# Kernel optimization log

Hardware: AMD Instinct MI355X
Metric: run time of the kernel (lower is better)

The kernel has to match this reference:

```python
import jax, jax.numpy as jnp
import numpy as np

NUM_EMBEDDINGS = 1024
EMBEDDING_DIM = 64
COMMITMENT_COST = 0.25


def setup_inputs() -> dict:
    key = jax.random.key(0)
    k_in, k_w = jax.random.split(key)
    inputs = jax.random.normal(k_in, (32, 64, 32, 32), dtype=jnp.float32)
    # nn.Embedding weight initialized uniform(-1/K, 1/K)
    bound = 1.0 / NUM_EMBEDDINGS
    weight = jax.random.uniform(k_w, (NUM_EMBEDDINGS, EMBEDDING_DIM),
                                dtype=jnp.float32, minval=-bound, maxval=bound)
    return {"inputs": inputs, "weight": weight}


def reference(inputs, weight):
    # Flatten to [N, D] rows in embedding space
    flat = inputs.reshape(-1, EMBEDDING_DIM)  # [N, D]
    distances = (jnp.sum(flat * flat, axis=1, keepdims=True)
                 + jnp.sum(weight * weight, axis=1)
                 - 2.0 * jnp.matmul(flat, weight.T))
    encoding_indices = jnp.argmin(distances, axis=1)  # [N]
    quantized = weight[encoding_indices].reshape(inputs.shape)
    e_latent_loss = jnp.mean((jax.lax.stop_gradient(quantized) - inputs) ** 2)
    q_latent_loss = jnp.mean((quantized - jax.lax.stop_gradient(inputs)) ** 2)
    commitment_loss = COMMITMENT_COST * (q_latent_loss + e_latent_loss)
    # Straight-through estimator
    quantized = inputs + jax.lax.stop_gradient(quantized - inputs)
    return quantized, encoding_indices[:, None], commitment_loss
```

## Files before the change

### kernel.cpp

```cpp
#include <hip/hip_runtime.h>

#define NROWS  32768
#define DIM    64
#define KCODES 1024
#define NELEM  (NROWS * DIM)
#define CHUNKS 16
#define CPC    (KCODES / CHUNKS)

typedef float v2f __attribute__((ext_vector_type(2)));

__device__ __forceinline__ float np_sumsq64(const float v[64]) {
#pragma clang fp contract(off)
  float r0 = v[0] * v[0];
  float r1 = v[1] * v[1];
  float r2 = v[2] * v[2];
  float r3 = v[3] * v[3];
  float r4 = v[4] * v[4];
  float r5 = v[5] * v[5];
  float r6 = v[6] * v[6];
  float r7 = v[7] * v[7];
#pragma unroll
  for (int i = 8; i < 64; i += 8) {
    r0 += v[i + 0] * v[i + 0];
    r1 += v[i + 1] * v[i + 1];
    r2 += v[i + 2] * v[i + 2];
    r3 += v[i + 3] * v[i + 3];
    r4 += v[i + 4] * v[i + 4];
    r5 += v[i + 5] * v[i + 5];
    r6 += v[i + 6] * v[i + 6];
    r7 += v[i + 7] * v[i + 7];
  }
  return ((r0 + r1) + (r2 + r3)) + ((r4 + r5) + (r6 + r7));
}

__global__ __launch_bounds__(256) void vq_prep(const float* __restrict__ x,
                                               const float* __restrict__ w,
                                               float* __restrict__ se,
                                               float* __restrict__ sxv,
                                               unsigned long long* __restrict__ keys) {
  const int t = blockIdx.x * 256 + threadIdx.x;
  keys[t] = ~0ull;

  float v[64];
  const float4* xr = (const float4*)(x + (size_t)t * DIM);
#pragma unroll
  for (int i = 0; i < 16; ++i) {
    float4 q = xr[i];
    v[4 * i + 0] = q.x; v[4 * i + 1] = q.y;
    v[4 * i + 2] = q.z; v[4 * i + 3] = q.w;
  }
  sxv[t] = np_sumsq64(v);

  if (t < KCODES) {
    const float4* wr = (const float4*)(w + (size_t)t * DIM);
#pragma unroll
    for (int i = 0; i < 16; ++i) {
      float4 q = wr[i];
      v[4 * i + 0] = q.x; v[4 * i + 1] = q.y;
      v[4 * i + 2] = q.z; v[4 * i + 3] = q.w;
    }
    se[t] = np_sumsq64(v);
  }
}

__global__ __launch_bounds__(256, 4) void vq_dist(const float* __restrict__ x,
                                                  const float* __restrict__ w,
                                                  const float* __restrict__ se,
                                                  const float* __restrict__ sxv,
                                                  unsigned long long* __restrict__ keys) {
  const int bid = blockIdx.x;
  const int l = (bid & 7) * (2048 / 8) + (bid >> 3);
  const int g = l >> 4;
  const int chunk = l & 15;
  const int row = g * 256 + threadIdx.x;

  v2f xv[32];
  const float4* xr = (const float4*)(x + (size_t)row * DIM);
#pragma unroll
  for (int i = 0; i < 16; ++i) {
    float4 t = xr[i];
    xv[2 * i + 0] = (v2f){t.x, t.y};
    xv[2 * i + 1] = (v2f){t.z, t.w};
  }
#pragma unroll
  for (int i = 0; i < 32; ++i) asm volatile("" : "+v"(xv[i]));
  const float sx = sxv[row];

  const int c0 = chunk * CPC;
  const float4* w4 = (const float4*)w;
  float bd = __builtin_inff();
  int bc = 0;

#pragma unroll 2
  for (int j = 0; j < CPC; ++j) {
    const int c = c0 + j;
    const float4* wr = w4 + (size_t)c * 16;
    v2f a0 = (v2f){0.f, 0.f}, a1 = (v2f){0.f, 0.f};
    v2f a2 = (v2f){0.f, 0.f}, a3 = (v2f){0.f, 0.f};
#pragma unroll
    for (int i = 0; i < 16; i += 2) {
      float4 t0 = wr[i];
      float4 t1 = wr[i + 1];
      a0 += (v2f){t0.x, t0.y} * xv[2 * i + 0];
      a1 += (v2f){t0.z, t0.w} * xv[2 * i + 1];
      a2 += (v2f){t1.x, t1.y} * xv[2 * i + 2];
      a3 += (v2f){t1.z, t1.w} * xv[2 * i + 3];
    }
    v2f s01 = a0 + a1;
    v2f s23 = a2 + a3;
    v2f s = s01 + s23;
    float dot = s.x + s.y;
    float d = fmaf(-2.0f, dot, sx + se[c]);
    if (d < bd) { bd = d; bc = c; }
  }

  unsigned long long key =
      ((unsigned long long)__float_as_uint(bd) << 32) | (unsigned long long)(unsigned)bc;
  atomicMin(&keys[row], key);
}

__global__ __launch_bounds__(256) void vq_out(const float* __restrict__ x,
                                              const float* __restrict__ w,
                                              const unsigned long long* __restrict__ keys,
                                              float* __restrict__ outq,
                                              float* __restrict__ outidx,
                                              double* __restrict__ part) {
  __shared__ int sidx[32];
  __shared__ double sp[4];
  const int b = blockIdx.x, t = threadIdx.x;

  if (t < 32) {
    const int row = b * 32 + t;
    unsigned long long k = keys[row];
    const int idx = (int)(unsigned int)(k & 0xFFFFFFFFull);
    outidx[row] = (float)idx;
    sidx[t] = idx;
  }
  __syncthreads();

  double acc = 0.0;
  const float4* x4 = (const float4*)x;
  float4* o4 = (float4*)outq;
#pragma unroll
  for (int i = 0; i < 2; ++i) {
    const int e = i * 256 + t;
    const int rl = e >> 4;
    const int d4 = e & 15;
    const size_t gofs = ((size_t)b * 32 + rl) * 16 + d4;
    float4 xvv = x4[gofs];
    const float4* wr = (const float4*)(w + (size_t)sidx[rl] * DIM);
    float4 wv = wr[d4];
    float tx = wv.x - xvv.x, ty = wv.y - xvv.y;
    float tz = wv.z - xvv.z, tw = wv.w - xvv.w;
    float4 q;
    q.x = xvv.x + tx; q.y = xvv.y + ty;
    q.z = xvv.z + tz; q.w = xvv.w + tw;
    o4[gofs] = q;
    acc += (double)tx * tx + (double)ty * ty + (double)tz * tz + (double)tw * tw;
  }

#pragma unroll
  for (int s = 32; s > 0; s >>= 1) acc += __shfl_down(acc, s, 64);
  if ((t & 63) == 0) sp[t >> 6] = acc;
  __syncthreads();
  if (t == 0) part[b] = (sp[0] + sp[1]) + (sp[2] + sp[3]);
}

__global__ __launch_bounds__(256) void vq_fin(const double* __restrict__ part,
                                              float* __restrict__ outloss) {
  __shared__ double sp[4];
  const int t = threadIdx.x;
  double a = (part[t] + part[t + 256]) + (part[t + 512] + part[t + 768]);
#pragma unroll
  for (int s = 32; s > 0; s >>= 1) a += __shfl_down(a, s, 64);
  if ((t & 63) == 0) sp[t >> 6] = a;
  __syncthreads();
  if (t == 0) {
    double total = (sp[0] + sp[1]) + (sp[2] + sp[3]);
    *outloss = 0.5f * (float)(total / (double)NELEM);
  }
}

extern "C" void kernel_launch(void* const* d_in, const int* in_sizes, int n_in,
                              void* d_out, int out_size, void* d_ws, size_t ws_size,
                              hipStream_t stream) {
  const float* x = (const float*)d_in[0];
  const float* w = (const float*)d_in[1];

  float* outq    = (float*)d_out;
  float* outidx  = outq + NELEM;
  float* outloss = outidx + NROWS;

  char* wsb = (char*)d_ws;
  float* se    = (float*)wsb;
  double* part = (double*)(wsb + 4096);
  float* sxv   = (float*)(wsb + 12288);
  unsigned long long* keys = (unsigned long long*)(wsb + 147456);

  hipLaunchKernelGGL(vq_prep, dim3(128),  dim3(256), 0, stream, x, w, se, sxv, keys);
  hipLaunchKernelGGL(vq_dist, dim3(2048), dim3(256), 0, stream, x, w, se, sxv, keys);
  hipLaunchKernelGGL(vq_out,  dim3(1024), dim3(256), 0, stream, x, w, keys, outq, outidx, part);
  hipLaunchKernelGGL(vq_fin,  dim3(1),    dim3(256), 0, stream, part, outloss);
}
```

Before: 126.0 us.

## Split each row across lane pairs in distance kernel and fuse loss finalization

The distance kernel now gives each row to two adjacent lanes, each holding half of the 64-dim vector, and combines the partial dot products with a DPP pair swap. This halves per-thread register use so launch bounds can allow 8 blocks per SIMD, and the codebook is cut into 8 chunks instead of 16 while keeping the same grid size. The separate final reduction kernel is dropped: each output block atomically adds its partial loss, and the last block, found with an atomic counter, writes the result. The trade-offs are an extra cross-lane op per code and a loss sum whose floating-point addition order is no longer fixed.

```diff
diff --git a/kernel.cpp b/kernel.cpp
--- a/kernel.cpp
+++ b/kernel.cpp
@@ -4,7 +4,7 @@
 #define DIM    64
 #define KCODES 1024
 #define NELEM  (NROWS * DIM)
-#define CHUNKS 16
+#define CHUNKS 8
 #define CPC    (KCODES / CHUNKS)
 
 typedef float v2f __attribute__((ext_vector_type(2)));
@@ -33,12 +33,20 @@
   return ((r0 + r1) + (r2 + r3)) + ((r4 + r5) + (r6 + r7));
 }
 
+__device__ __forceinline__ float swap_pair(float v) {
+  return __int_as_float(
+      __builtin_amdgcn_mov_dpp(__float_as_int(v), 0xB1, 0xF, 0xF, true));
+}
+
 __global__ __launch_bounds__(256) void vq_prep(const float* __restrict__ x,
                                                const float* __restrict__ w,
                                                float* __restrict__ se,
                                                float* __restrict__ sxv,
-                                               unsigned long long* __restrict__ keys) {
+                                               unsigned long long* __restrict__ keys,
+                                               double* __restrict__ loss,
+                                               unsigned int* __restrict__ cnt) {
   const int t = blockIdx.x * 256 + threadIdx.x;
+  if (t == 0) { *loss = 0.0; *cnt = 0u; }
   keys[t] = ~0ull;
 
   float v[64];
@@ -63,60 +71,62 @@
   }
 }
 
-__global__ __launch_bounds__(256, 4) void vq_dist(const float* __restrict__ x,
+__global__ __launch_bounds__(256, 8) void vq_dist(const float* __restrict__ x,
                                                   const float* __restrict__ w,
                                                   const float* __restrict__ se,
                                                   const float* __restrict__ sxv,
                                                   unsigned long long* __restrict__ keys) {
   const int bid = blockIdx.x;
-  const int l = (bid & 7) * (2048 / 8) + (bid >> 3);
-  const int g = l >> 4;
-  const int chunk = l & 15;
-  const int row = g * 256 + threadIdx.x;
-
-  v2f xv[32];
+  const int xcd = bid & 7;
+  const int j = bid >> 3;
+  const int chunk = (j >> 3) & 7;
+  const int group = (xcd << 5) + (j & 7) + ((j >> 6) << 3);
+  const int t = threadIdx.x;
+  const int h = t & 1;
+  const int row = group * 128 + (t >> 1);
+
+  v2f xh[16];
   const float4* xr = (const float4*)(x + (size_t)row * DIM);
 #pragma unroll
-  for (int i = 0; i < 16; ++i) {
-    float4 t = xr[i];
-    xv[2 * i + 0] = (v2f){t.x, t.y};
-    xv[2 * i + 1] = (v2f){t.z, t.w};
-  }
-#pragma unroll
-  for (int i = 0; i < 32; ++i) asm volatile("" : "+v"(xv[i]));
+  for (int k = 0; k < 8; ++k) {
+    float4 q = xr[2 * k + h];
+    xh[2 * k + 0] = (v2f){q.x, q.y};
+    xh[2 * k + 1] = (v2f){q.z, q.w};
+  }
+#pragma unroll
+  for (int i = 0; i < 16; ++i) asm volatile("" : "+v"(xh[i]));
   const float sx = sxv[row];
 
   const int c0 = chunk * CPC;
-  const float4* w4 = (const float4*)w;
   float bd = __builtin_inff();
   int bc = 0;
 
 #pragma unroll 2
-  for (int j = 0; j < CPC; ++j) {
-    const int c = c0 + j;
-    const float4* wr = w4 + (size_t)c * 16;
-    v2f a0 = (v2f){0.f, 0.f}, a1 = (v2f){0.f, 0.f};
-    v2f a2 = (v2f){0.f, 0.f}, a3 = (v2f){0.f, 0.f};
-#pragma unroll
-    for (int i = 0; i < 16; i += 2) {
-      float4 t0 = wr[i];
-      float4 t1 = wr[i + 1];
-      a0 += (v2f){t0.x, t0.y} * xv[2 * i + 0];
-      a1 += (v2f){t0.z, t0.w} * xv[2 * i + 1];
-      a2 += (v2f){t1.x, t1.y} * xv[2 * i + 2];
-      a3 += (v2f){t1.z, t1.w} * xv[2 * i + 3];
+  for (int jj = 0; jj < CPC; ++jj) {
+    const int c = c0 + jj;
+    const float4* wr = (const float4*)(w + (size_t)c * DIM) + h;
+    v2f aA = (v2f){0.f, 0.f}, aB = (v2f){0.f, 0.f};
+#pragma unroll
+    for (int k = 0; k < 8; ++k) {
+      float4 q = wr[2 * k];
+      aA += (v2f){q.x, q.y} * xh[2 * k + 0];
+      aB += (v2f){q.z, q.w} * xh[2 * k + 1];
     }
-    v2f s01 = a0 + a1;
-    v2f s23 = a2 + a3;
-    v2f s = s01 + s23;
+    v2f mine = aA + aB;
+    v2f oth;
+    oth.x = swap_pair(mine.x);
+    oth.y = swap_pair(mine.y);
+    v2f s = mine + oth;
     float dot = s.x + s.y;
     float d = fmaf(-2.0f, dot, sx + se[c]);
     if (d < bd) { bd = d; bc = c; }
   }
 
-  unsigned long long key =
-      ((unsigned long long)__float_as_uint(bd) << 32) | (unsigned long long)(unsigned)bc;
-  atomicMin(&keys[row], key);
+  if (h == 0) {
+    unsigned long long key =
+        ((unsigned long long)__float_as_uint(bd) << 32) | (unsigned long long)(unsigned)bc;
+    atomicMin(&keys[row], key);
+  }
 }
 
 __global__ __launch_bounds__(256) void vq_out(const float* __restrict__ x,
@@ -124,7 +134,9 @@
                                               const unsigned long long* __restrict__ keys,
                                               float* __restrict__ outq,
                                               float* __restrict__ outidx,
-                                              double* __restrict__ part) {
+                                              double* __restrict__ loss,
+                                              unsigned int* __restrict__ cnt,
+                                              float* __restrict__ outloss) {
   __shared__ int sidx[32];
   __shared__ double sp[4];
   const int b = blockIdx.x, t = threadIdx.x;
@@ -163,21 +175,14 @@
   for (int s = 32; s > 0; s >>= 1) acc += __shfl_down(acc, s, 64);
   if ((t & 63) == 0) sp[t >> 6] = acc;
   __syncthreads();
-  if (t == 0) part[b] = (sp[0] + sp[1]) + (sp[2] + sp[3]);
-}
-
-__global__ __launch_bounds__(256) void vq_fin(const double* __restrict__ part,
-                                              float* __restrict__ outloss) {
-  __shared__ double sp[4];
-  const int t = threadIdx.x;
-  double a = (part[t] + part[t + 256]) + (part[t + 512] + part[t + 768]);
-#pragma unroll
-  for (int s = 32; s > 0; s >>= 1) a += __shfl_down(a, s, 64);
-  if ((t & 63) == 0) sp[t >> 6] = a;
-  __syncthreads();
   if (t == 0) {
-    double total = (sp[0] + sp[1]) + (sp[2] + sp[3]);
-    *outloss = 0.5f * (float)(total / (double)NELEM);
+    atomicAdd(loss, (sp[0] + sp[1]) + (sp[2] + sp[3]));
+    __threadfence();
+    unsigned int old = atomicAdd(cnt, 1u);
+    if (old == 1023u) {
+      double total = atomicAdd(loss, 0.0);
+      *outloss = 0.5f * (float)(total / (double)NELEM);
+    }
   }
 }
 
@@ -192,13 +197,13 @@
   float* outloss = outidx + NROWS;
 
   char* wsb = (char*)d_ws;
-  float* se    = (float*)wsb;
-  double* part = (double*)(wsb + 4096);
-  float* sxv   = (float*)(wsb + 12288);
+  double* loss      = (double*)wsb;
+  unsigned int* cnt = (unsigned int*)(wsb + 64);
+  float* se    = (float*)(wsb + 256);
+  float* sxv   = (float*)(wsb + 8192);
   unsigned long long* keys = (unsigned long long*)(wsb + 147456);
 
-  hipLaunchKernelGGL(vq_prep, dim3(128),  dim3(256), 0, stream, x, w, se, sxv, keys);
+  hipLaunchKernelGGL(vq_prep, dim3(128),  dim3(256), 0, stream, x, w, se, sxv, keys, loss, cnt);
   hipLaunchKernelGGL(vq_dist, dim3(2048), dim3(256), 0, stream, x, w, se, sxv, keys);
-  hipLaunchKernelGGL(vq_out,  dim3(1024), dim3(256), 0, stream, x, w, keys, outq, outidx, part);
-  hipLaunchKernelGGL(vq_fin,  dim3(1),    dim3(256), 0, stream, part, outloss);
-}
+  hipLaunchKernelGGL(vq_out,  dim3(1024), dim3(256), 0, stream, x, w, keys, outq, outidx, loss, cnt, outloss);
+}
```

New measurement: 339.8 us. +169.7%, slower.
